# Optimization experiments

Measured on AMD Instinct MI355X. Metric: run time of the kernel, lower is better.

The kernel has to match this reference:

```python
import jax, jax.numpy as jnp
import numpy as np

IN_F = 512
OUT_F = 256
N = 8192
ALPHA = 0.2  # LeakyReLU negative slope
NEG_BIG = -9e15


def setup_inputs() -> dict:
    key = jax.random.key(0)
    k1, k2, k3, k4 = jax.random.split(key, 4)
    x = jax.random.normal(k1, (N, IN_F), dtype=jnp.float32)
    adj = jax.random.randint(k2, (N, N), 0, 2, dtype=jnp.int32)
    # Xavier-uniform-like params
    limW = float(np.sqrt(6.0 / (IN_F + OUT_F)))
    W = jax.random.uniform(k3, (IN_F, OUT_F), jnp.float32, -limW, limW)
    lima = float(np.sqrt(6.0 / (2 * OUT_F + 1)))
    a = jax.random.uniform(k4, (2 * OUT_F, 1), jnp.float32, -lima, lima)
    bias = jnp.zeros((OUT_F,), jnp.float32)
    return {"x": x, "adj": adj, "W": W, "a": a, "bias": bias}


def reference(x, adj, W, a, bias):
    h = x @ W  # (N, OUT_F)
    # Additive attention score e_ij = leakyrelu(a1.h_i + a2.h_j)
    # (same math as the NxNx2F concat in the original, without materializing it)
    a1 = a[:OUT_F, 0]
    a2 = a[OUT_F:, 0]
    s1 = h @ a1  # (N,)
    s2 = h @ a2  # (N,)
    e = jax.nn.leaky_relu(s1[:, None] + s2[None, :], negative_slope=ALPHA)  # (N, N)
    e = jnp.where(adj > 0, e, NEG_BIG)
    attention = jax.nn.softmax(e, axis=1)  # dropout is identity in eval mode
    h_prime = attention @ h + bias
    return h_prime
```

## Files before the change

### kernel.cpp

```cpp
#include <hip/hip_runtime.h>

#define NN 8192
#define INF_ 512
#define OUTF 256
#define LOG2E 1.4426950408889634f

typedef __attribute__((ext_vector_type(8))) short short8;
typedef __attribute__((ext_vector_type(4))) float f4;
typedef __attribute__((ext_vector_type(4))) int i4;

__device__ __forceinline__ unsigned short f2bf(float f) {
  union { float f; unsigned u; } v; v.f = f;
  unsigned r = v.u + 0x7fffu + ((v.u >> 16) & 1u);
  return (unsigned short)(r >> 16);
}
__device__ __forceinline__ float bf2f(unsigned short h) {
  union { unsigned u; float f; } v; v.u = ((unsigned)h) << 16;
  return v.f;
}

__global__ void k_wsplit(const float* __restrict__ W, unsigned short* __restrict__ Whi,
                         unsigned short* __restrict__ Wlo) {
  int idx = blockIdx.x * 256 + threadIdx.x;
  int k = idx >> 8, c = idx & 255;
  float w = W[idx];
  unsigned short hi = f2bf(w);
  unsigned short lo = f2bf(w - bf2f(hi));
  Whi[c * INF_ + k] = hi;
  Wlo[c * INF_ + k] = lo;
}

__global__ void __launch_bounds__(64) k_h(
    const float* __restrict__ x, const float* __restrict__ a,
    const unsigned short* __restrict__ Whi, const unsigned short* __restrict__ Wlo,
    unsigned short* __restrict__ hT, float* __restrict__ s1, float* __restrict__ s2) {
  const int rowbase = blockIdx.x * 16;
  const int l = threadIdx.x;
  const int r15 = l & 15, kg = l >> 4;

  f4 acc[16];
#pragma unroll
  for (int i = 0; i < 16; ++i) acc[i] = (f4){0.f, 0.f, 0.f, 0.f};

  for (int kk = 0; kk < INF_; kk += 32) {
    const float* xp = x + (rowbase + r15) * INF_ + kk + kg * 8;
    f4 xa = *(const f4*)xp;
    f4 xb = *(const f4*)(xp + 4);
    short8 ahi, alo;
#pragma unroll
    for (int e = 0; e < 8; ++e) {
      float f = (e < 4) ? xa[e] : xb[e - 4];
      unsigned short h = f2bf(f);
      ahi[e] = (short)h;
      alo[e] = (short)f2bf(f - bf2f(h));
    }
#pragma unroll
    for (int cg = 0; cg < 16; ++cg) {
      int col = cg * 16 + r15;
      const short8 bhi = *(const short8*)(Whi + col * INF_ + kk + kg * 8);
      const short8 blo = *(const short8*)(Wlo + col * INF_ + kk + kg * 8);
      acc[cg] = __builtin_amdgcn_mfma_f32_16x16x32_bf16(ahi, bhi, acc[cg], 0, 0, 0);
      acc[cg] = __builtin_amdgcn_mfma_f32_16x16x32_bf16(ahi, blo, acc[cg], 0, 0, 0);
      acc[cg] = __builtin_amdgcn_mfma_f32_16x16x32_bf16(alo, bhi, acc[cg], 0, 0, 0);
    }
  }
  float sp1[4] = {0, 0, 0, 0}, sp2[4] = {0, 0, 0, 0};
#pragma unroll
  for (int cg = 0; cg < 16; ++cg) {
    int col = cg * 16 + r15;
    float a1v = a[col] * LOG2E, a2v = a[OUTF + col] * LOG2E;
#pragma unroll
    for (int r = 0; r < 4; ++r) {
      float v = acc[cg][r];
      hT[col * NN + rowbase + kg * 4 + r] = f2bf(v);
      sp1[r] += v * a1v;
      sp2[r] += v * a2v;
    }
  }
#pragma unroll
  for (int r = 0; r < 4; ++r) {
#pragma unroll
    for (int m = 1; m < 16; m <<= 1) {
      sp1[r] += __shfl_xor(sp1[r], m, 16);
      sp2[r] += __shfl_xor(sp2[r], m, 16);
    }
    if (r15 == 0) {
      s1[rowbase + kg * 4 + r] = sp1[r];
      s2[rowbase + kg * 4 + r] = sp2[r];
    }
  }
}

__global__ void __launch_bounds__(256, 2) k_attn(
    const int* __restrict__ adj, const float* __restrict__ s1G,
    const float* __restrict__ s2G, const unsigned short* __restrict__ hT,
    float* __restrict__ accG, float* __restrict__ lG) {
  __shared__ int adjb[3][4096];
  __shared__ unsigned short wbuf[4096];
  __shared__ float s2l[2048];

  const int b = blockIdx.x;
  const int chunk = b & 3;
  const int rowbase = (b >> 2) * 64;
  const int jchunk = chunk * 2048;
  const int tid = threadIdx.x;
  const int wv = tid >> 6;
  const int l = tid & 63;
  const int r15 = l & 15, kg = l >> 4;
  const int row_w = wv * 16 + r15;
  const int colbase = wv * 64;

  const float s1v = s1G[rowbase + row_w];

  {
    const float* sp = s2G + jchunk + tid * 8;
    f4 v0 = *(const f4*)sp;
    f4 v1 = *(const f4*)(sp + 4);
    *(f4*)&s2l[tid * 8] = v0;
    *(f4*)&s2l[tid * 8 + 4] = v1;
  }
#pragma unroll
  for (int p = 0; p < 2; ++p) {
    const int jn = jchunk + p * 64;
#pragma unroll
    for (int q = 0; q < 4; ++q) {
      const int row_t = (wv * 4 + q) * 4 + kg;
      const int s = r15 ^ (row_t & 15);
      const int* src = adj + (rowbase + row_t) * NN + jn + s * 4;
      __builtin_amdgcn_global_load_lds(
          (const __attribute__((address_space(1))) unsigned int*)src,
          (__attribute__((address_space(3))) unsigned int*)&adjb[p][(wv * 4 + q) * 256], 16, 0, 0);
    }
  }
  asm volatile("s_waitcnt lgkmcnt(0)" ::: "memory");
  __builtin_amdgcn_s_barrier();

  f4 acc[4][4];
#pragma unroll
  for (int rg = 0; rg < 4; ++rg)
#pragma unroll
    for (int cg = 0; cg < 4; ++cg) acc[rg][cg] = (f4){0.f, 0.f, 0.f, 0.f};
  float lsum = 0.f;

  for (int t = 0; t < 32; ++t) {
    const int jt = jchunk + t * 64;
    short8 bfr[2][4];
#pragma unroll
    for (int ks = 0; ks < 2; ++ks)
#pragma unroll
      for (int cg = 0; cg < 4; ++cg)
        bfr[ks][cg] = *(const short8*)(hT + (colbase + cg * 16 + r15) * NN + jt + ks * 32 + kg * 8);
    {
      const int tn = (t + 2 <= 31) ? t + 2 : 31;
      const int slot = (t + 2) % 3;
      const int jn = jchunk + tn * 64;
#pragma unroll
      for (int q = 0; q < 4; ++q) {
        const int row_t = (wv * 4 + q) * 4 + kg;
        const int s = r15 ^ (row_t & 15);
        const int* src = adj + (rowbase + row_t) * NN + jn + s * 4;
        __builtin_amdgcn_global_load_lds(
            (const __attribute__((address_space(1))) unsigned int*)src,
            (__attribute__((address_space(3))) unsigned int*)&adjb[slot][(wv * 4 + q) * 256], 16, 0, 0);
      }
    }
    if (t == 0) asm volatile("s_waitcnt vmcnt(12)" ::: "memory");
    else        asm volatile("s_waitcnt vmcnt(24)" ::: "memory");
    const int slotc = t % 3;
    i4 av[4];
#pragma unroll
    for (int k = 0; k < 4; ++k)
      av[k] = *(const i4*)&adjb[slotc][row_w * 64 + (((kg * 4 + k) ^ (row_w & 15)) << 2)];
    f4 s2v[4];
#pragma unroll
    for (int k = 0; k < 4; ++k)
      s2v[k] = *(const f4*)&s2l[t * 64 + kg * 16 + k * 4];
    unsigned short wp[16];
#pragma unroll
    for (int k = 0; k < 4; ++k)
#pragma unroll
      for (int e2 = 0; e2 < 4; ++e2) {
        float xx = s1v + s2v[k][e2];
        float lr = fmaxf(xx, 0.2f * xx);
        float pp = __builtin_amdgcn_exp2f(lr);
        float w0 = (av[k][e2] > 0) ? pp : 0.0f;
        unsigned short hh = f2bf(w0);
        wp[k * 4 + e2] = hh;
        lsum += bf2f(hh);
      }
    short8 w0p, w1p;
#pragma unroll
    for (int e = 0; e < 8; ++e) { w0p[e] = (short)wp[e]; w1p[e] = (short)wp[8 + e]; }
    *(short8*)&wbuf[row_w * 64 + (((kg * 2) ^ (row_w & 7)) << 3)] = w0p;
    *(short8*)&wbuf[row_w * 64 + (((kg * 2 + 1) ^ (row_w & 7)) << 3)] = w1p;
    asm volatile("s_waitcnt lgkmcnt(0)" ::: "memory");
    __builtin_amdgcn_s_barrier();
    short8 afr[2][4];
#pragma unroll
    for (int ks = 0; ks < 2; ++ks)
#pragma unroll
      for (int rg = 0; rg < 4; ++rg) {
        const int rr = rg * 16 + r15;
        afr[ks][rg] = *(const short8*)&wbuf[rr * 64 + (((ks * 4 + kg) ^ (rr & 7)) << 3)];
      }
#pragma unroll
    for (int ks = 0; ks < 2; ++ks)
#pragma unroll
      for (int rg = 0; rg < 4; ++rg)
#pragma unroll
        for (int cg = 0; cg < 4; ++cg)
          acc[rg][cg] = __builtin_amdgcn_mfma_f32_16x16x32_bf16(afr[ks][rg], bfr[ks][cg], acc[rg][cg], 0, 0, 0);
    __builtin_amdgcn_s_barrier();
  }

  lsum += __shfl_xor(lsum, 16, 64);
  lsum += __shfl_xor(lsum, 32, 64);
  if (kg == 0) atomicAdd(&lG[rowbase + row_w], lsum);
#pragma unroll
  for (int rg = 0; rg < 4; ++rg)
#pragma unroll
    for (int cg = 0; cg < 4; ++cg)
#pragma unroll
      for (int r = 0; r < 4; ++r)
        atomicAdd(&accG[(rowbase + rg * 16 + kg * 4 + r) * OUTF + colbase + cg * 16 + r15],
                  acc[rg][cg][r]);
}

__global__ void k_final(const float* __restrict__ accG, const float* __restrict__ lG,
                        const float* __restrict__ bias, float* __restrict__ out) {
  int idx = blockIdx.x * 256 + threadIdx.x;
  int row = idx >> 6;
  int c4 = idx & 63;
  f4 v = ((const f4*)accG)[idx];
  float inv = 1.0f / lG[row];
  f4 bb = ((const f4*)bias)[c4];
  f4 o;
#pragma unroll
  for (int e = 0; e < 4; ++e) o[e] = v[e] * inv + bb[e];
  ((f4*)out)[idx] = o;
}

extern "C" void kernel_launch(void* const* d_in, const int* in_sizes, int n_in,
                              void* d_out, int out_size, void* d_ws, size_t ws_size,
                              hipStream_t stream) {
  const float* x = (const float*)d_in[0];
  const int* adj = (const int*)d_in[1];
  const float* W = (const float*)d_in[2];
  const float* a = (const float*)d_in[3];
  const float* bias = (const float*)d_in[4];
  float* out = (float*)d_out;

  char* ws = (char*)d_ws;
  float* accG = (float*)(ws);
  float* lG   = (float*)(ws + 8388608);
  unsigned short* hT  = (unsigned short*)(ws + 8421376);
  unsigned short* Whi = (unsigned short*)(ws + 12615680);
  unsigned short* Wlo = (unsigned short*)(ws + 12877824);
  float* s1 = (float*)(ws + 13139968);
  float* s2 = (float*)(ws + 13172736);

  hipMemsetAsync(accG, 0, 8421376, stream);
  k_wsplit<<<512, 256, 0, stream>>>(W, Whi, Wlo);
  k_h<<<512, 64, 0, stream>>>(x, a, Whi, Wlo, hT, s1, s2);
  k_attn<<<512, 256, 0, stream>>>(adj, s1, s2, hT, accG, lG);
  k_final<<<2048, 256, 0, stream>>>(accG, lG, bias, out);
}
```

Measured before the change: 204.3 us.

## Split attention into weight-generation pass and separate bf16 GEMM with split-K partials

```diff
diff --git a/kernel.cpp b/kernel.cpp
--- a/kernel.cpp
+++ b/kernel.cpp
@@ -6,6 +6,7 @@
 #define LOG2E 1.4426950408889634f
 
 typedef __attribute__((ext_vector_type(8))) short short8;
+typedef __attribute__((ext_vector_type(4))) short short4v;
 typedef __attribute__((ext_vector_type(4))) float f4;
 typedef __attribute__((ext_vector_type(4))) int i4;
 
@@ -91,152 +92,139 @@
   }
 }
 
-__global__ void __launch_bounds__(256, 2) k_attn(
+__global__ void __launch_bounds__(256) k_wgen(
     const int* __restrict__ adj, const float* __restrict__ s1G,
-    const float* __restrict__ s2G, const unsigned short* __restrict__ hT,
-    float* __restrict__ accG, float* __restrict__ lG) {
-  __shared__ int adjb[3][4096];
-  __shared__ unsigned short wbuf[4096];
-  __shared__ float s2l[2048];
-
+    const float* __restrict__ s2G, unsigned short* __restrict__ w,
+    float* __restrict__ lG) {
+  __shared__ float red[4];
+  const int row = blockIdx.x;
+  const int tid = threadIdx.x;
+  const float s1v = s1G[row];
+  const i4* ap = (const i4*)(adj + (size_t)row * NN);
+  const f4* sp = (const f4*)s2G;
+  unsigned short* wrow = w + (size_t)row * NN;
+  float lsum = 0.f;
+
+#pragma unroll
+  for (int u = 0; u < 8; ++u) {
+    const int q = u * 256 + tid;
+    i4 m = ap[q];
+    f4 sv = sp[q];
+    short4v wp;
+#pragma unroll
+    for (int e = 0; e < 4; ++e) {
+      float xx = s1v + sv[e];
+      float lr = fmaxf(xx, 0.2f * xx);
+      float pp = __builtin_amdgcn_exp2f(lr);
+      float w0 = (m[e] > 0) ? pp : 0.0f;
+      unsigned short hh = f2bf(w0);
+      wp[e] = (short)hh;
+      lsum += bf2f(hh);
+    }
+    *(short4v*)(wrow + q * 4) = wp;
+  }
+
+#pragma unroll
+  for (int m = 1; m < 64; m <<= 1) lsum += __shfl_xor(lsum, m, 64);
+  if ((tid & 63) == 0) red[tid >> 6] = lsum;
+  __syncthreads();
+  if (tid == 0) lG[row] = red[0] + red[1] + red[2] + red[3];
+}
+
+__global__ void __launch_bounds__(256) k_av(
+    const unsigned short* __restrict__ w, const unsigned short* __restrict__ hT,
+    float* __restrict__ CP) {
+  __shared__ unsigned short At[2][8192];
   const int b = blockIdx.x;
-  const int chunk = b & 3;
-  const int rowbase = (b >> 2) * 64;
-  const int jchunk = chunk * 2048;
+  const int rt = b >> 2, qt = b & 3;
+  const int rowbase = rt * 64;
+  const int kbase = qt * 2048;
   const int tid = threadIdx.x;
-  const int wv = tid >> 6;
-  const int l = tid & 63;
+  const int wv = tid >> 6, l = tid & 63;
   const int r15 = l & 15, kg = l >> 4;
-  const int row_w = wv * 16 + r15;
   const int colbase = wv * 64;
-
-  const float s1v = s1G[rowbase + row_w];
-
-  {
-    const float* sp = s2G + jchunk + tid * 8;
-    f4 v0 = *(const f4*)sp;
-    f4 v1 = *(const f4*)(sp + 4);
-    *(f4*)&s2l[tid * 8] = v0;
-    *(f4*)&s2l[tid * 8 + 4] = v1;
-  }
-#pragma unroll
-  for (int p = 0; p < 2; ++p) {
-    const int jn = jchunk + p * 64;
-#pragma unroll
-    for (int q = 0; q < 4; ++q) {
-      const int row_t = (wv * 4 + q) * 4 + kg;
-      const int s = r15 ^ (row_t & 15);
-      const int* src = adj + (rowbase + row_t) * NN + jn + s * 4;
-      __builtin_amdgcn_global_load_lds(
-          (const __attribute__((address_space(1))) unsigned int*)src,
-          (__attribute__((address_space(3))) unsigned int*)&adjb[p][(wv * 4 + q) * 256], 16, 0, 0);
-    }
-  }
-  asm volatile("s_waitcnt lgkmcnt(0)" ::: "memory");
+  const char* wb = (const char*)w;
+
+#define STAGE_A(buf, t)                                                           \
+  {                                                                               \
+    _Pragma("unroll")                                                             \
+    for (int q = 0; q < 4; ++q) {                                                 \
+      const int d = q * 4096 + tid * 16;                    \
+      const int r = d >> 8;                                         \
+      const int cb = d & 255;                                    \
+      const int sc = cb ^ ((r & 7) << 4);          \
+      const char* src = wb + (size_t)(rowbase + r) * (NN * 2) +                   \
+                        (size_t)(kbase + (t) * 128) * 2 + sc;                     \
+      __builtin_amdgcn_global_load_lds(                                           \
+          (const __attribute__((address_space(1))) unsigned int*)src,             \
+          (__attribute__((address_space(3))) unsigned int*)                       \
+              ((char*)&At[buf][0] + d), 16, 0, 0);                                \
+    }                                                                             \
+  }
+
+  f4 acc[4][4];
+#pragma unroll
+  for (int rg = 0; rg < 4; ++rg)
+#pragma unroll
+    for (int cg = 0; cg < 4; ++cg) acc[rg][cg] = (f4){0.f, 0.f, 0.f, 0.f};
+
+  STAGE_A(0, 0)
+  asm volatile("s_waitcnt vmcnt(0)" ::: "memory");
   __builtin_amdgcn_s_barrier();
 
-  f4 acc[4][4];
+  int cur = 0;
+  for (int t = 0; t < 16; ++t) {
+    short8 Bf[4][4];
+#pragma unroll
+    for (int ks = 0; ks < 4; ++ks)
+#pragma unroll
+      for (int cg = 0; cg < 4; ++cg)
+        Bf[ks][cg] = *(const short8*)(hT + (size_t)(colbase + cg * 16 + r15) * NN +
+                                      kbase + t * 128 + ks * 32 + kg * 8);
+    if (t < 15) STAGE_A(cur ^ 1, t + 1)
+#pragma unroll
+    for (int ks = 0; ks < 4; ++ks)
+#pragma unroll
+      for (int rg = 0; rg < 4; ++rg) {
+        const int r = rg * 16 + r15;
+        const int byte = ((r * 256 + ks * 64 + kg * 16) ^ ((r & 7) << 4));
+        const short8 Af = *(const short8*)((const char*)&At[cur][0] + byte);
+#pragma unroll
+        for (int cg = 0; cg < 4; ++cg)
+          acc[rg][cg] = __builtin_amdgcn_mfma_f32_16x16x32_bf16(Af, Bf[ks][cg], acc[rg][cg], 0, 0, 0);
+      }
+    asm volatile("s_waitcnt vmcnt(0)" ::: "memory");
+    __builtin_amdgcn_s_barrier();
+    cur ^= 1;
+  }
+
+  float* cp = CP + (size_t)qt * NN * OUTF;
 #pragma unroll
   for (int rg = 0; rg < 4; ++rg)
 #pragma unroll
-    for (int cg = 0; cg < 4; ++cg) acc[rg][cg] = (f4){0.f, 0.f, 0.f, 0.f};
-  float lsum = 0.f;
-
-  for (int t = 0; t < 32; ++t) {
-    const int jt = jchunk + t * 64;
-    short8 bfr[2][4];
-#pragma unroll
-    for (int ks = 0; ks < 2; ++ks)
-#pragma unroll
-      for (int cg = 0; cg < 4; ++cg)
-        bfr[ks][cg] = *(const short8*)(hT + (colbase + cg * 16 + r15) * NN + jt + ks * 32 + kg * 8);
-    {
-      const int tn = (t + 2 <= 31) ? t + 2 : 31;
-      const int slot = (t + 2) % 3;
-      const int jn = jchunk + tn * 64;
-#pragma unroll
-      for (int q = 0; q < 4; ++q) {
-        const int row_t = (wv * 4 + q) * 4 + kg;
-        const int s = r15 ^ (row_t & 15);
-        const int* src = adj + (rowbase + row_t) * NN + jn + s * 4;
-        __builtin_amdgcn_global_load_lds(
-            (const __attribute__((address_space(1))) unsigned int*)src,
-            (__attribute__((address_space(3))) unsigned int*)&adjb[slot][(wv * 4 + q) * 256], 16, 0, 0);
-      }
-    }
-    if (t == 0) asm volatile("s_waitcnt vmcnt(12)" ::: "memory");
-    else        asm volatile("s_waitcnt vmcnt(24)" ::: "memory");
-    const int slotc = t % 3;
-    i4 av[4];
-#pragma unroll
-    for (int k = 0; k < 4; ++k)
-      av[k] = *(const i4*)&adjb[slotc][row_w * 64 + (((kg * 4 + k) ^ (row_w & 15)) << 2)];
-    f4 s2v[4];
-#pragma unroll
-    for (int k = 0; k < 4; ++k)
-      s2v[k] = *(const f4*)&s2l[t * 64 + kg * 16 + k * 4];
-    unsigned short wp[16];
-#pragma unroll
-    for (int k = 0; k < 4; ++k)
-#pragma unroll
-      for (int e2 = 0; e2 < 4; ++e2) {
-        float xx = s1v + s2v[k][e2];
-        float lr = fmaxf(xx, 0.2f * xx);
-        float pp = __builtin_amdgcn_exp2f(lr);
-        float w0 = (av[k][e2] > 0) ? pp : 0.0f;
-        unsigned short hh = f2bf(w0);
-        wp[k * 4 + e2] = hh;
-        lsum += bf2f(hh);
-      }
-    short8 w0p, w1p;
-#pragma unroll
-    for (int e = 0; e < 8; ++e) { w0p[e] = (short)wp[e]; w1p[e] = (short)wp[8 + e]; }
-    *(short8*)&wbuf[row_w * 64 + (((kg * 2) ^ (row_w & 7)) << 3)] = w0p;
-    *(short8*)&wbuf[row_w * 64 + (((kg * 2 + 1) ^ (row_w & 7)) << 3)] = w1p;
-    asm volatile("s_waitcnt lgkmcnt(0)" ::: "memory");
-    __builtin_amdgcn_s_barrier();
-    short8 afr[2][4];
-#pragma unroll
-    for (int ks = 0; ks < 2; ++ks)
-#pragma unroll
-      for (int rg = 0; rg < 4; ++rg) {
-        const int rr = rg * 16 + r15;
-        afr[ks][rg] = *(const short8*)&wbuf[rr * 64 + (((ks * 4 + kg) ^ (rr & 7)) << 3)];
-      }
-#pragma unroll
-    for (int ks = 0; ks < 2; ++ks)
-#pragma unroll
-      for (int rg = 0; rg < 4; ++rg)
-#pragma unroll
-        for (int cg = 0; cg < 4; ++cg)
-          acc[rg][cg] = __builtin_amdgcn_mfma_f32_16x16x32_bf16(afr[ks][rg], bfr[ks][cg], acc[rg][cg], 0, 0, 0);
-    __builtin_amdgcn_s_barrier();
-  }
-
-  lsum += __shfl_xor(lsum, 16, 64);
-  lsum += __shfl_xor(lsum, 32, 64);
-  if (kg == 0) atomicAdd(&lG[rowbase + row_w], lsum);
-#pragma unroll
-  for (int rg = 0; rg < 4; ++rg)
-#pragma unroll
     for (int cg = 0; cg < 4; ++cg)
 #pragma unroll
       for (int r = 0; r < 4; ++r)
-        atomicAdd(&accG[(rowbase + rg * 16 + kg * 4 + r) * OUTF + colbase + cg * 16 + r15],
-                  acc[rg][cg][r]);
-}
-
-__global__ void k_final(const float* __restrict__ accG, const float* __restrict__ lG,
+        cp[(size_t)(rowbase + rg * 16 + kg * 4 + r) * OUTF + colbase + cg * 16 + r15] =
+            acc[rg][cg][r];
+}
+
+__global__ void k_final(const float* __restrict__ CP, const float* __restrict__ lG,
                         const float* __restrict__ bias, float* __restrict__ out) {
-  int idx = blockIdx.x * 256 + threadIdx.x;
-  int row = idx >> 6;
-  int c4 = idx & 63;
-  f4 v = ((const f4*)accG)[idx];
+  const int idx = blockIdx.x * 256 + threadIdx.x;
+  const int row = idx >> 6;
+  const int c4 = idx & 63;
+  const int CS = NN * OUTF / 4;
+  f4 v0 = ((const f4*)CP)[idx];
+  f4 v1 = ((const f4*)CP)[idx + CS];
+  f4 v2 = ((const f4*)CP)[idx + 2 * CS];
+  f4 v3 = ((const f4*)CP)[idx + 3 * CS];
   float inv = 1.0f / lG[row];
   f4 bb = ((const f4*)bias)[c4];
   f4 o;
 #pragma unroll
-  for (int e = 0; e < 4; ++e) o[e] = v[e] * inv + bb[e];
+  for (int e = 0; e < 4; ++e)
+    o[e] = (v0[e] + v1[e] + v2[e] + v3[e]) * inv + bb[e];
   ((f4*)out)[idx] = o;
 }
 
@@ -251,17 +239,18 @@
   float* out = (float*)d_out;
 
   char* ws = (char*)d_ws;
-  float* accG = (float*)(ws);
-  float* lG   = (float*)(ws + 8388608);
-  unsigned short* hT  = (unsigned short*)(ws + 8421376);
-  unsigned short* Whi = (unsigned short*)(ws + 12615680);
-  unsigned short* Wlo = (unsigned short*)(ws + 12877824);
-  float* s1 = (float*)(ws + 13139968);
-  float* s2 = (float*)(ws + 13172736);
-
-  hipMemsetAsync(accG, 0, 8421376, stream);
+  unsigned short* w  = (unsigned short*)(ws);
+  float* CP  = (float*)(ws + 134217728);
+  float* lG  = (float*)(ws + 167772160);
+  unsigned short* hT  = (unsigned short*)(ws + 167804928);
+  unsigned short* Whi = (unsigned short*)(ws + 171999232);
+  unsigned short* Wlo = (unsigned short*)(ws + 172261376);
+  float* s1 = (float*)(ws + 172523520);
+  float* s2 = (float*)(ws + 172556288);
+
   k_wsplit<<<512, 256, 0, stream>>>(W, Whi, Wlo);
   k_h<<<512, 64, 0, stream>>>(x, a, Whi, Wlo, hT, s1, s2);
-  k_attn<<<512, 256, 0, stream>>>(adj, s1, s2, hT, accG, lG);
-  k_final<<<2048, 256, 0, stream>>>(accG, lG, bias, out);
-}
+  k_wgen<<<8192, 256, 0, stream>>>(adj, s1, s2, w, lG);
+  k_av<<<512, 256, 0, stream>>>(w, hT, CP);
+  k_final<<<2048, 256, 0, stream>>>(CP, lG, bias, out);
+}
```

New measurement: 252.7 us. 23.7% more time.
